# Performance work log

Hardware: AMD Instinct MI355X
Metric: run time of the kernel (lower is better)

Reference implementation:

```python
import jax, jax.numpy as jnp
import numpy as np

B, L, H, E = 4, 2048, 8, 64  # S == L

def setup_inputs() -> dict:
    key = jax.random.key(0)
    k1, k2, k3, k4, k5 = jax.random.split(key, 5)
    q = jax.random.normal(k1, (B, L, H, E), dtype=jnp.float32)
    k = jax.random.normal(k2, (B, L, H, E), dtype=jnp.float32)
    v = jax.random.normal(k3, (B, L, H, E), dtype=jnp.float32)
    tau = jax.random.uniform(k4, (B, 1), dtype=jnp.float32) + 0.5  # positive scale
    delta = jax.random.normal(k5, (B, L), dtype=jnp.float32) * 0.1
    return {"q": q, "k": k, "v": v, "tau": tau, "delta": delta}

def reference(q, k, v, tau, delta):
    # De-stationarized attention: scores = (QK^T) * tau + delta, softmax(scale*scores)
    E_ = q.shape[-1]
    scale = 1.0 / jnp.sqrt(jnp.float32(E_))
    # tau: [B,1] -> [B,1,1,1]; delta: [B,S] -> [B,1,1,S]
    scores = jnp.einsum('blhe,bshe->bhls', q, k) * tau[:, None, None] + delta[:, None, None, :]
    a = jax.nn.softmax(scale * scores, axis=-1)  # dropout is identity in eval / p=0
    out = jnp.einsum('bhls,bshd->blhd', a, v)
    return out, a
```

## Files before the change

kernel.cpp:

```cpp
#include <hip/hip_runtime.h>
#include <stdint.h>

#define B_ 4
#define L_ 2048
#define H_ 8
#define E_ 64
#define S_ 2048

typedef __bf16 bf16x8 __attribute__((ext_vector_type(8)));
typedef _Float16 f16x8 __attribute__((ext_vector_type(8)));
typedef _Float16 f16x4 __attribute__((ext_vector_type(4)));
typedef float f32x4 __attribute__((ext_vector_type(4)));
typedef unsigned short u16;
typedef u16 u16x4 __attribute__((ext_vector_type(4)));

__device__ __forceinline__ u16 f32_to_bf16(float f) {
  union { float f; uint32_t u; } x;
  x.f = f;
  uint32_t u = x.u;
  return (u16)((u + 0x7FFFu + ((u >> 16) & 1u)) >> 16);
}

__global__ __launch_bounds__(256) void prep_qkd(
    const float* __restrict__ q, const float* __restrict__ k,
    const float* __restrict__ tau, const float* __restrict__ delta,
    u16* __restrict__ qb, u16* __restrict__ kb, float* __restrict__ dl) {
  int idx = blockIdx.x * 256 + threadIdx.x;
  int i4 = idx * 4;
  int b = i4 >> 20;
  const float C = 0.125f * 1.44269504088896f;
  float ts = tau[b] * C;
  f32x4 qv = *(const f32x4*)(q + i4);
  f32x4 kv = *(const f32x4*)(k + i4);
  u16x4 qs, ks;
#pragma unroll
  for (int j = 0; j < 4; ++j) {
    qs[j] = f32_to_bf16(qv[j] * ts);
    ks[j] = f32_to_bf16(kv[j]);
  }
  *(u16x4*)(qb + i4) = qs;
  *(u16x4*)(kb + i4) = ks;
  if (idx < (B_ * S_) / 4) {
    f32x4 dv = *(const f32x4*)(delta + i4);
    f32x4 ds = {dv[0] * C, dv[1] * C, dv[2] * C, dv[3] * C};
    *(f32x4*)(dl + i4) = ds;
  }
}

__global__ __launch_bounds__(256) void prep_v(const float* __restrict__ v,
                                              u16* __restrict__ vb) {
  __shared__ float t[32][33];
  int bid = blockIdx.x;
  int et = bid & 1;
  int st = (bid >> 1) & 63;
  int h = (bid >> 7) & 7;
  int b = bid >> 10;
  int tx = threadIdx.x & 31;
  int ty = threadIdx.x >> 5;
#pragma unroll
  for (int k2 = 0; k2 < 4; ++k2) {
    int s = st * 32 + ty + 8 * k2;
    int e = et * 32 + tx;
    t[ty + 8 * k2][tx] = v[(((size_t)b * S_ + s) * H_ + h) * E_ + e];
  }
  __syncthreads();
#pragma unroll
  for (int k2 = 0; k2 < 4; ++k2) {
    int e = et * 32 + ty + 8 * k2;
    int s = st * 32 + tx;
    _Float16 hf = (_Float16)t[tx][ty + 8 * k2];
    vb[(((size_t)b * H_ + h) * E_ + e) * S_ + s] = __builtin_bit_cast(u16, hf);
  }
}

__global__ __launch_bounds__(256, 2) void attn_fused(
    const u16* __restrict__ qb, const u16* __restrict__ kb,
    const u16* __restrict__ vbuf, const float* __restrict__ dl,
    float* __restrict__ out, float* __restrict__ oa) {
  __shared__ __align__(16) u16 sc[16 * 2048];
  __shared__ float psum[4][16];

  int bid = blockIdx.x;
  int swz = (bid & 7) * 512 + (bid >> 3);
  int b = swz >> 10;
  int h = (swz >> 7) & 7;
  int qt = swz & 127;
  int m0 = qt * 16;
  int tid = threadIdx.x, lane = tid & 63, wave = tid >> 6;
  int l15 = lane & 15, l4 = lane >> 4;
  int s0 = wave * 512;
  int xm = (l15 & 7) << 4;
  char* scb = (char*)sc;

  const u16* qp = qb + (((size_t)b * L_ + (m0 + l15)) * H_ + h) * E_ + 8 * l4;
  bf16x8 qa0 = *(const bf16x8*)qp;
  bf16x8 qa1 = *(const bf16x8*)(qp + 32);

  const u16* kbase = kb + (((size_t)b * S_ + (s0 + l15)) * H_ + h) * E_ + 8 * l4;
  const float* dbase = dl + b * S_ + s0 + 4 * l4;

  float sums = 0.f;
#pragma unroll 4
  for (int t = 0; t < 32; ++t) {
    const u16* kp = kbase + (size_t)t * (16 * H_ * E_);
    bf16x8 ka0 = *(const bf16x8*)kp;
    bf16x8 ka1 = *(const bf16x8*)(kp + 32);
    f32x4 dv = *(const f32x4*)(dbase + 16 * t);
    f32x4 acc = {0.f, 0.f, 0.f, 0.f};
    acc = __builtin_amdgcn_mfma_f32_16x16x32_bf16(ka0, qa0, acc, 0, 0, 0);
    acc = __builtin_amdgcn_mfma_f32_16x16x32_bf16(ka1, qa1, acc, 0, 0, 0);
    float p0 = __builtin_amdgcn_exp2f(acc[0] + dv[0]);
    float p1 = __builtin_amdgcn_exp2f(acc[1] + dv[1]);
    float p2 = __builtin_amdgcn_exp2f(acc[2] + dv[2]);
    float p3 = __builtin_amdgcn_exp2f(acc[3] + dv[3]);
    sums += (p0 + p1) + (p2 + p3);
    f16x4 pv = {(_Float16)p0, (_Float16)p1, (_Float16)p2, (_Float16)p3};
    int off = (l15 << 12) + (((s0 << 1) + (t << 5) + (l4 << 3)) ^ xm);
    *(f16x4*)(scb + off) = pv;
  }
  sums += __shfl_xor(sums, 16, 64);
  sums += __shfl_xor(sums, 32, 64);
  if (lane < 16) psum[wave][lane] = sums;
  __syncthreads();

  const u16* vb0 =
      vbuf + ((size_t)(b * H_ + h) * E_ + 16 * wave + l15) * S_ + 8 * l4;
  f32x4 oaccA = {0.f, 0.f, 0.f, 0.f};
  f32x4 oaccB = {0.f, 0.f, 0.f, 0.f};
#pragma unroll 4
  for (int c = 0; c < 64; c += 2) {
    f16x8 af0 = *(const f16x8*)(scb + (l15 << 12) + (((c << 6) + (l4 << 4)) ^ xm));
    f16x8 vf0 = *(const f16x8*)(vb0 + (c << 5));
    oaccA = __builtin_amdgcn_mfma_f32_16x16x32_f16(af0, vf0, oaccA, 0, 0, 0);
    f16x8 af1 = *(const f16x8*)(scb + (l15 << 12) + ((((c + 1) << 6) + (l4 << 4)) ^ xm));
    f16x8 vf1 = *(const f16x8*)(vb0 + ((c + 1) << 5));
    oaccB = __builtin_amdgcn_mfma_f32_16x16x32_f16(af1, vf1, oaccB, 0, 0, 0);
  }

#pragma unroll
  for (int r = 0; r < 4; ++r) {
    int row = 4 * l4 + r;
    float zr = 1.f / (psum[0][row] + psum[1][row] + psum[2][row] + psum[3][row]);
    float o = oaccA[r] + oaccB[r];
    out[(((size_t)b * L_ + (m0 + row)) * H_ + h) * E_ + 16 * wave + l15] = o * zr;
  }

  {
    int row = 4 * wave + l4;
    float zrow =
        1.f / (psum[0][row] + psum[1][row] + psum[2][row] + psum[3][row]);
    float* ar = oa + (((size_t)(b * H_ + h)) * L_ + (m0 + row)) * S_;
    int xr = (row & 7) << 4;
    const char* scr = scb + (row << 12);
#pragma unroll 4
    for (int it = 0; it < 16; ++it) {
      f16x8 pv = *(const f16x8*)(scr + (((it << 8) + (l15 << 4)) ^ xr));
      f32x4 lo = {(float)pv[0] * zrow, (float)pv[1] * zrow,
                  (float)pv[2] * zrow, (float)pv[3] * zrow};
      f32x4 hi = {(float)pv[4] * zrow, (float)pv[5] * zrow,
                  (float)pv[6] * zrow, (float)pv[7] * zrow};
      int col = it * 128 + l15 * 8;
      *(f32x4*)(ar + col) = lo;
      *(f32x4*)(ar + col + 4) = hi;
    }
  }
}

extern "C" void kernel_launch(void* const* d_in, const int* in_sizes, int n_in,
                              void* d_out, int out_size, void* d_ws, size_t ws_size,
                              hipStream_t stream) {
  (void)in_sizes; (void)n_in; (void)out_size;
  const float* q = (const float*)d_in[0];
  const float* k = (const float*)d_in[1];
  const float* v = (const float*)d_in[2];
  const float* tau = (const float*)d_in[3];
  const float* delta = (const float*)d_in[4];
  float* out = (float*)d_out;
  float* oa = out + (size_t)B_ * L_ * H_ * E_;

  const size_t NQ = (size_t)B_ * L_ * H_ * E_;
  u16* qb = (u16*)d_ws;
  u16* kb = qb + NQ;
  u16* vb = kb + NQ;
  float* dl = (float*)(vb + NQ);
  size_t need = 3 * NQ * sizeof(u16) + (size_t)B_ * S_ * sizeof(float);
  if (ws_size < need) return;

  prep_qkd<<<4096, 256, 0, stream>>>(q, k, tau, delta, qb, kb, dl);
  prep_v<<<4096, 256, 0, stream>>>(v, vb);
  attn_fused<<<4096, 256, 0, stream>>>(qb, kb, vb, dl, out, oa);
}
```

Baseline: 347.3 us.

## Double attention block to 512 threads with split-K PV and LDS reduction

```diff
diff --git a/kernel.cpp b/kernel.cpp
--- a/kernel.cpp
+++ b/kernel.cpp
@@ -73,12 +73,13 @@
   }
 }
 
-__global__ __launch_bounds__(256, 2) void attn_fused(
+__global__ __launch_bounds__(512, 4) void attn_fused(
     const u16* __restrict__ qb, const u16* __restrict__ kb,
     const u16* __restrict__ vbuf, const float* __restrict__ dl,
     float* __restrict__ out, float* __restrict__ oa) {
   __shared__ __align__(16) u16 sc[16 * 2048];
-  __shared__ float psum[4][16];
+  __shared__ float psum[8][16];
+  __shared__ float ox[4][16][17];
 
   int bid = blockIdx.x;
   int swz = (bid & 7) * 512 + (bid >> 3);
@@ -88,7 +89,7 @@
   int m0 = qt * 16;
   int tid = threadIdx.x, lane = tid & 63, wave = tid >> 6;
   int l15 = lane & 15, l4 = lane >> 4;
-  int s0 = wave * 512;
+  int s0 = wave * 256;
   int xm = (l15 & 7) << 4;
   char* scb = (char*)sc;
 
@@ -101,7 +102,7 @@
 
   float sums = 0.f;
 #pragma unroll 4
-  for (int t = 0; t < 32; ++t) {
+  for (int t = 0; t < 16; ++t) {
     const u16* kp = kbase + (size_t)t * (16 * H_ * E_);
     bf16x8 ka0 = *(const bf16x8*)kp;
     bf16x8 ka1 = *(const bf16x8*)(kp + 32);
@@ -123,43 +124,61 @@
   if (lane < 16) psum[wave][lane] = sums;
   __syncthreads();
 
-  const u16* vb0 =
-      vbuf + ((size_t)(b * H_ + h) * E_ + 16 * wave + l15) * S_ + 8 * l4;
-  f32x4 oaccA = {0.f, 0.f, 0.f, 0.f};
-  f32x4 oaccB = {0.f, 0.f, 0.f, 0.f};
+  float zq[2];
+
+  {
+    int et = wave & 3;
+    int h2 = wave >> 2;
+    const u16* vb0 =
+        vbuf + ((size_t)(b * H_ + h) * E_ + 16 * et + l15) * S_ + h2 * 1024 + 8 * l4;
+    const char* sch = scb + (l15 << 12) + (h2 << 11);
+    f32x4 oaccA = {0.f, 0.f, 0.f, 0.f};
+    f32x4 oaccB = {0.f, 0.f, 0.f, 0.f};
 #pragma unroll 4
-  for (int c = 0; c < 64; c += 2) {
-    f16x8 af0 = *(const f16x8*)(scb + (l15 << 12) + (((c << 6) + (l4 << 4)) ^ xm));
-    f16x8 vf0 = *(const f16x8*)(vb0 + (c << 5));
-    oaccA = __builtin_amdgcn_mfma_f32_16x16x32_f16(af0, vf0, oaccA, 0, 0, 0);
-    f16x8 af1 = *(const f16x8*)(scb + (l15 << 12) + ((((c + 1) << 6) + (l4 << 4)) ^ xm));
-    f16x8 vf1 = *(const f16x8*)(vb0 + ((c + 1) << 5));
-    oaccB = __builtin_amdgcn_mfma_f32_16x16x32_f16(af1, vf1, oaccB, 0, 0, 0);
-  }
-
-#pragma unroll
-  for (int r = 0; r < 4; ++r) {
-    int row = 4 * l4 + r;
-    float zr = 1.f / (psum[0][row] + psum[1][row] + psum[2][row] + psum[3][row]);
-    float o = oaccA[r] + oaccB[r];
-    out[(((size_t)b * L_ + (m0 + row)) * H_ + h) * E_ + 16 * wave + l15] = o * zr;
+    for (int c = 0; c < 32; c += 2) {
+      f16x8 af0 = *(const f16x8*)(sch + (((c << 6) + (l4 << 4)) ^ xm));
+      f16x8 vf0 = *(const f16x8*)(vb0 + (c << 5));
+      oaccA = __builtin_amdgcn_mfma_f32_16x16x32_f16(af0, vf0, oaccA, 0, 0, 0);
+      f16x8 af1 = *(const f16x8*)(sch + ((((c + 1) << 6) + (l4 << 4)) ^ xm));
+      f16x8 vf1 = *(const f16x8*)(vb0 + ((c + 1) << 5));
+      oaccB = __builtin_amdgcn_mfma_f32_16x16x32_f16(af1, vf1, oaccB, 0, 0, 0);
+    }
+    oaccA += oaccB;
+    if (h2 == 1) {
+#pragma unroll
+      for (int r = 0; r < 4; ++r) ox[et][4 * l4 + r][l15] = oaccA[r];
+    }
+    __syncthreads();
+    if (h2 == 0) {
+#pragma unroll
+      for (int r = 0; r < 4; ++r) {
+        int row = 4 * l4 + r;
+        float zr = psum[0][row] + psum[1][row] + psum[2][row] + psum[3][row] +
+                   psum[4][row] + psum[5][row] + psum[6][row] + psum[7][row];
+        float o = oaccA[r] + ox[et][row][l15];
+        out[(((size_t)b * L_ + (m0 + row)) * H_ + h) * E_ + 16 * et + l15] =
+            o / zr;
+      }
+    }
   }
 
   {
-    int row = 4 * wave + l4;
-    float zrow =
-        1.f / (psum[0][row] + psum[1][row] + psum[2][row] + psum[3][row]);
+    int row = 2 * wave + (lane >> 5);
+    int l31 = lane & 31;
+    float zrow = psum[0][row] + psum[1][row] + psum[2][row] + psum[3][row] +
+                 psum[4][row] + psum[5][row] + psum[6][row] + psum[7][row];
+    float zi = 1.f / zrow;
     float* ar = oa + (((size_t)(b * H_ + h)) * L_ + (m0 + row)) * S_;
     int xr = (row & 7) << 4;
     const char* scr = scb + (row << 12);
 #pragma unroll 4
-    for (int it = 0; it < 16; ++it) {
-      f16x8 pv = *(const f16x8*)(scr + (((it << 8) + (l15 << 4)) ^ xr));
-      f32x4 lo = {(float)pv[0] * zrow, (float)pv[1] * zrow,
-                  (float)pv[2] * zrow, (float)pv[3] * zrow};
-      f32x4 hi = {(float)pv[4] * zrow, (float)pv[5] * zrow,
-                  (float)pv[6] * zrow, (float)pv[7] * zrow};
-      int col = it * 128 + l15 * 8;
+    for (int it = 0; it < 8; ++it) {
+      f16x8 pv = *(const f16x8*)(scr + (((it << 9) + (l31 << 4)) ^ xr));
+      f32x4 lo = {(float)pv[0] * zi, (float)pv[1] * zi,
+                  (float)pv[2] * zi, (float)pv[3] * zi};
+      f32x4 hi = {(float)pv[4] * zi, (float)pv[5] * zi,
+                  (float)pv[6] * zi, (float)pv[7] * zi};
+      int col = it * 256 + l31 * 8;
       *(f32x4*)(ar + col) = lo;
       *(f32x4*)(ar + col + 4) = hi;
     }
@@ -188,5 +207,5 @@
 
   prep_qkd<<<4096, 256, 0, stream>>>(q, k, tau, delta, qb, kb, dl);
   prep_v<<<4096, 256, 0, stream>>>(v, vb);
-  attn_fused<<<4096, 256, 0, stream>>>(qb, kb, vb, dl, out, oa);
-}
+  attn_fused<<<4096, 512, 0, stream>>>(qb, kb, vb, dl, out, oa);
+}
```

Result: no change. 341.9 us (-1.6%).
